# Kernel optimization log

Hardware: AMD Instinct MI355X
Metric: run time of the kernel (lower is better)

## Reference

```python
import jax, jax.numpy as jnp
import numpy as np

INPUT_SIZE = 1024  # enc_dim + dec_dim after concat
ENC_DIM = 512
DEC_DIM = 512
INNER_DIM = 512
VOCAB = 2048


def setup_inputs() -> dict:
    key = jax.random.key(0)
    k1, k2, k3, k4, k5, k6 = jax.random.split(key, 6)
    B, T, U = 4, 256, 128
    enc_state = jax.random.normal(k1, (B, T, ENC_DIM), dtype=jnp.float32)
    dec_state = jax.random.normal(k2, (B, U, DEC_DIM), dtype=jnp.float32)
    # forward_layer: Linear(input_size, inner_dim); stored as [in, out] for jax
    s1 = 1.0 / np.sqrt(INPUT_SIZE)
    W1 = jax.random.uniform(k3, (INPUT_SIZE, INNER_DIM), jnp.float32, -s1, s1)
    b1 = jax.random.uniform(k4, (INNER_DIM,), jnp.float32, -s1, s1)
    s2 = 1.0 / np.sqrt(INNER_DIM)
    W2 = jax.random.uniform(k5, (INNER_DIM, VOCAB), jnp.float32, -s2, s2)
    b2 = jax.random.uniform(k6, (VOCAB,), jnp.float32, -s2, s2)
    return {"enc_state": enc_state, "dec_state": dec_state,
            "W1": W1, "b1": b1, "W2": W2, "b2": b2}


def reference(enc_state, dec_state, W1, b1, W2, b2):
    # JointNet: concat(enc_repeat, dec_repeat) @ W1 + b1 -> tanh -> @ W2 + b2.
    # Since W1 acts on the concat axis, split it: concat @ W1 == enc @ W1_e + dec @ W1_d
    # (mathematically identical, avoids materializing the [B,T,U,2D] concat tensor).
    W1_enc = W1[:ENC_DIM]   # [D_enc, inner]
    W1_dec = W1[ENC_DIM:]   # [D_dec, inner]
    enc_proj = jnp.einsum('btd,dh->bth', enc_state, W1_enc)  # [B,T,H]
    dec_proj = jnp.einsum('bud,dh->buh', dec_state, W1_dec)  # [B,U,H]
    h = jnp.tanh(enc_proj[:, :, None, :] + dec_proj[:, None, :, :] + b1)  # [B,T,U,H]
    logits = jnp.einsum('btuh,hv->btuv', h, W2) + b2  # [B,T,U,V]
    return logits
```

## Files before the change

kernel.cpp:

```cpp
#include <hip/hip_runtime.h>
#include <hip/hip_bf16.h>


typedef __attribute__((ext_vector_type(4))) float f32x4;
typedef __attribute__((ext_vector_type(8))) __bf16 bf16x8;
typedef __attribute__((ext_vector_type(8))) unsigned short u16x8;

__device__ __forceinline__ float bf2f(unsigned short u) {
  unsigned int x = ((unsigned int)u) << 16;
  return __builtin_bit_cast(float, x);
}
__device__ __forceinline__ unsigned short f2bf(float f) {
  unsigned int x = __builtin_bit_cast(unsigned int, f);
  x += 0x7fff + ((x >> 16) & 1);
  return (unsigned short)(x >> 16);
}
__device__ __forceinline__ float tanh_fast(float x) {
  float e = __expf(2.0f * x);
  return 1.0f - 2.0f * __builtin_amdgcn_rcpf(e + 1.0f);
}

typedef __attribute__((address_space(3))) unsigned int lds_u32;
typedef const __attribute__((address_space(1))) unsigned int glb_u32;
__device__ __forceinline__ void gl16(const void* g, void* l) {
  __builtin_amdgcn_global_load_lds((glb_u32*)g, (lds_u32*)l, 16, 0, 0);
}

#define BAR __builtin_amdgcn_s_barrier()
#define LGKM0 asm volatile("s_waitcnt lgkmcnt(0)" ::: "memory")
#define VMCNT(n) asm volatile("s_waitcnt vmcnt(" #n ")" ::: "memory")
#define MEMPIN asm volatile("" ::: "memory")

__global__ __launch_bounds__(512) void proj8_kernel(
    const float* __restrict__ enc, const float* __restrict__ dec,
    const float* __restrict__ W1, const float* __restrict__ b1,
    float* __restrict__ enc_proj, unsigned short* __restrict__ decb) {
  __shared__ float xs[8][512];
  const int bid = blockIdx.x;
  const bool isenc = bid < 128;
  const int rows0 = (isenc ? bid : bid - 128) * 8;
  const float* src = (isenc ? enc : dec) + (size_t)rows0 * 512;
  const int tid = threadIdx.x;
#pragma unroll
  for (int j = 0; j < 2; ++j) {
    int v = j * 512 + tid;
    int row = v >> 7;
    int c4 = (v & 127) << 2;
    *(f32x4*)&xs[row][c4] = *(const f32x4*)&src[(size_t)row * 512 + c4];
  }
  __syncthreads();
  const int h = tid;
  const float* wp = W1 + (isenc ? 0 : (size_t)512 * 512) + h;
  float acc[8];
  float init = isenc ? 0.f : b1[h];
#pragma unroll
  for (int r = 0; r < 8; ++r) acc[r] = init;
#pragma unroll 4
  for (int k = 0; k < 512; ++k) {
    float wv = wp[(size_t)k * 512];
#pragma unroll
    for (int r = 0; r < 8; ++r) acc[r] = fmaf(xs[r][k], wv, acc[r]);
  }
  if (isenc) {
#pragma unroll
    for (int r = 0; r < 8; ++r) enc_proj[(size_t)(rows0 + r) * 512 + h] = acc[r];
  } else {
#pragma unroll
    for (int r = 0; r < 8; ++r) decb[(size_t)(rows0 + r) * 512 + h] = f2bf(acc[r]);
  }
}

__global__ __launch_bounds__(256) void w2t_kernel(const float* __restrict__ W2,
                                                  unsigned short* __restrict__ W2t) {
  __shared__ unsigned short tile[32][33];
  int bn = blockIdx.x;
  int bk = blockIdx.y;
  int tx = threadIdx.x & 31;
  int ty = threadIdx.x >> 5;
#pragma unroll
  for (int i = 0; i < 32; i += 8)
    tile[ty + i][tx] = f2bf(W2[(size_t)(bk * 32 + ty + i) * 2048 + bn * 32 + tx]);
  __syncthreads();
#pragma unroll
  for (int i = 0; i < 32; i += 8)
    W2t[(size_t)(bn * 32 + ty + i) * 512 + bk * 32 + tx] = tile[tx][ty + i];
}

__global__ __launch_bounds__(256) void h_kernel(
    const float* __restrict__ encp, const unsigned short* __restrict__ decb,
    unsigned short* __restrict__ Hout) {
  int gid = blockIdx.x * 256 + threadIdx.x;
  int m = gid >> 6;
  int hc = (gid & 63) << 3;
  int bt = m >> 7;
  int bu = ((m >> 15) << 7) | (m & 127);
  u16x8 dv = *(const u16x8*)(decb + (size_t)bu * 512 + hc);
  f32x4 e0 = *(const f32x4*)(encp + (size_t)bt * 512 + hc);
  f32x4 e1 = *(const f32x4*)(encp + (size_t)bt * 512 + hc + 4);
  u16x8 hv;
#pragma unroll
  for (int j = 0; j < 4; ++j) hv[j] = f2bf(tanh_fast(bf2f(dv[j]) + e0[j]));
#pragma unroll
  for (int j = 0; j < 4; ++j) hv[4 + j] = f2bf(tanh_fast(bf2f(dv[4 + j]) + e1[j]));
  *(u16x8*)(Hout + (size_t)m * 512 + hc) = hv;
}


__global__ __launch_bounds__(512, 4) void gemm32_kernel(
    const unsigned short* __restrict__ H,
    const unsigned short* __restrict__ W2t,
    const float* __restrict__ b2,
    float* __restrict__ out) {
  __shared__ __align__(1024) char smem[73728];

  const int bid = blockIdx.x;
  const int wg = (bid & 7) * 1024 + (bid >> 3);
  const int my = wg >> 3;
  const int ny = wg & 7;

  const int tid = threadIdx.x;
  const int lane = tid & 63;
  const int w = tid >> 6;
  const int wm = w >> 2;
  const int wn = w & 3;
  const int fr = lane & 15;
  const int fq = lane >> 4;

  const char* ha = (const char*)(H + (size_t)my * 128 * 512);
  const char* wb = (const char*)(W2t + (size_t)ny * 256 * 512);

  size_t srcA, srcB[2];
  {
    int d = w * 1024 + lane * 16;
    int r = d >> 6;
    int c = (d >> 4) & 3;
    srcA = (size_t)r * 1024 + (size_t)((c ^ ((r >> 1) & 3)) << 4);
  }
#pragma unroll
  for (int p = 0; p < 2; ++p) {
    int d = p * 8192 + w * 1024 + lane * 16;
    int r = d >> 6;
    int c = (d >> 4) & 3;
    srcB[p] = (size_t)r * 1024 + (size_t)((c ^ ((r >> 1) & 3)) << 4);
  }

  const int swz = (fq ^ ((fr >> 1) & 3)) << 4;
  const int ldsA = (wm * 64 + fr) * 64 + swz;
  const int ldsB = 8192 + (wn * 64 + fr) * 64 + swz;

  f32x4 acc[4][4];
#pragma unroll
  for (int i = 0; i < 4; ++i)
#pragma unroll
    for (int j = 0; j < 4; ++j) acc[i][j] = (f32x4){0.f, 0.f, 0.f, 0.f};

#define STAGE(tt, slot)                                         \
  do {                                                          \
    char* sl = smem + (slot)*24576;                             \
    gl16(ha + srcA + (tt)*64, sl + w * 1024);                   \
    gl16(wb + srcB[0] + (tt)*64, sl + 8192 + w * 1024);         \
    gl16(wb + srcB[1] + (tt)*64, sl + 16384 + w * 1024);        \
  } while (0)

  STAGE(0, 0);
  STAGE(1, 1);

#pragma unroll
  for (int t = 0; t < 16; ++t) {
    if (t < 15) { VMCNT(3); } else { VMCNT(0); }
    BAR; MEMPIN;
    const char* As = smem + (t % 3) * 24576;
    bf16x8 a4[4], b4[4];
#pragma unroll
    for (int mi = 0; mi < 4; ++mi) a4[mi] = *(const bf16x8*)(As + ldsA + mi * 1024);
#pragma unroll
    for (int ni = 0; ni < 4; ++ni) b4[ni] = *(const bf16x8*)(As + ldsB + ni * 1024);
    if (t + 2 < 16) STAGE(t + 2, (t + 2) % 3);
    LGKM0;
    __builtin_amdgcn_s_setprio(1);
#pragma unroll
    for (int mi = 0; mi < 4; ++mi)
#pragma unroll
      for (int ni = 0; ni < 4; ++ni)
        acc[mi][ni] = __builtin_amdgcn_mfma_f32_16x16x32_bf16(
            a4[mi], b4[ni], acc[mi][ni], 0, 0, 0);
    __builtin_amdgcn_s_setprio(0);
  }
  BAR; MEMPIN;

  float* lbuf = (float*)smem;
  const size_t orow0 = (size_t)my * 128;
  const int ncol0 = ny * 256;
  float bvv[4];
#pragma unroll
  for (int ni = 0; ni < 4; ++ni) bvv[ni] = b2[ncol0 + wn * 64 + ni * 16 + fr];

#pragma unroll
  for (int c = 0; c < 8; ++c) {
    if ((c >> 2) == wm) {
      const int mi = c & 3;
#pragma unroll
      for (int ni = 0; ni < 4; ++ni)
#pragma unroll
        for (int r = 0; r < 4; ++r)
          lbuf[(fq * 4 + r) * 260 + wn * 64 + ni * 16 + fr] =
              acc[mi][ni][r] + bvv[ni];
    }
    LGKM0; BAR; MEMPIN;
#pragma unroll
    for (int rr = 0; rr < 2; ++rr) {
      const int row = w * 2 + rr;
      f32x4 v = *(const f32x4*)&lbuf[row * 260 + lane * 4];
      __builtin_nontemporal_store(
          v, (f32x4*)&out[(orow0 + c * 16 + row) * 2048 + ncol0 + lane * 4]);
    }
    LGKM0; BAR; MEMPIN;
  }
#undef STAGE
}

extern "C" void kernel_launch(void* const* d_in, const int* in_sizes, int n_in,
                              void* d_out, int out_size, void* d_ws, size_t ws_size,
                              hipStream_t stream) {
  const float* enc = (const float*)d_in[0];
  const float* dec = (const float*)d_in[1];
  const float* W1  = (const float*)d_in[2];
  const float* b1  = (const float*)d_in[3];
  const float* W2  = (const float*)d_in[4];
  const float* b2  = (const float*)d_in[5];
  float* out = (float*)d_out;

  char* ws = (char*)d_ws;
  float* enc_proj = (float*)ws;
  unsigned short* decb = (unsigned short*)(ws + (2u << 20));
  unsigned short* W2t  = (unsigned short*)(ws + (2u << 20) + (512u << 10));
  unsigned short* Hbuf = (unsigned short*)(ws + (8u << 20));

  proj8_kernel<<<192, 512, 0, stream>>>(enc, dec, W1, b1, enc_proj, decb);
  w2t_kernel<<<dim3(64, 16), 256, 0, stream>>>(W2, W2t);
  h_kernel<<<32768, 256, 0, stream>>>(enc_proj, decb, Hbuf);
  gemm32_kernel<<<8192, 512, 0, stream>>>(Hbuf, W2t, b2, out);
}
```

Before: 398.7 us.

## Fuse tanh activation into GEMM A-tile production, dropping the H intermediate

Removes the separate h_kernel and the 128 MB bf16 H buffer. The GEMM now builds each A tile in LDS itself: it loads decoder-projection rows from global memory, adds the encoder-projection row cached in LDS, applies tanh, and packs the result to bf16. Register prefetch of the decoder rows is pipelined alongside the existing B-tile async loads, which cuts HBM traffic for writing and re-reading H. In exchange the GEMM's inner loop carries extra transcendental ALU work and register pressure, and the output stores change from nontemporal to regular stores.

```diff
diff --git a/kernel.cpp b/kernel.cpp
--- a/kernel.cpp
+++ b/kernel.cpp
@@ -5,6 +5,7 @@
 typedef __attribute__((ext_vector_type(4))) float f32x4;
 typedef __attribute__((ext_vector_type(8))) __bf16 bf16x8;
 typedef __attribute__((ext_vector_type(8))) unsigned short u16x8;
+typedef __attribute__((ext_vector_type(4))) unsigned int u32x4;
 
 __device__ __forceinline__ float bf2f(unsigned short u) {
   unsigned int x = ((unsigned int)u) << 16;
@@ -18,6 +19,9 @@
 __device__ __forceinline__ float tanh_fast(float x) {
   float e = __expf(2.0f * x);
   return 1.0f - 2.0f * __builtin_amdgcn_rcpf(e + 1.0f);
+}
+__device__ __forceinline__ unsigned int pk2bf(float lo, float hi) {
+  return (unsigned int)f2bf(lo) | ((unsigned int)f2bf(hi) << 16);
 }
 
 typedef __attribute__((address_space(3))) unsigned int lds_u32;
@@ -86,32 +90,14 @@
     W2t[(size_t)(bn * 32 + ty + i) * 512 + bk * 32 + tx] = tile[tx][ty + i];
 }
 
-__global__ __launch_bounds__(256) void h_kernel(
-    const float* __restrict__ encp, const unsigned short* __restrict__ decb,
-    unsigned short* __restrict__ Hout) {
-  int gid = blockIdx.x * 256 + threadIdx.x;
-  int m = gid >> 6;
-  int hc = (gid & 63) << 3;
-  int bt = m >> 7;
-  int bu = ((m >> 15) << 7) | (m & 127);
-  u16x8 dv = *(const u16x8*)(decb + (size_t)bu * 512 + hc);
-  f32x4 e0 = *(const f32x4*)(encp + (size_t)bt * 512 + hc);
-  f32x4 e1 = *(const f32x4*)(encp + (size_t)bt * 512 + hc + 4);
-  u16x8 hv;
-#pragma unroll
-  for (int j = 0; j < 4; ++j) hv[j] = f2bf(tanh_fast(bf2f(dv[j]) + e0[j]));
-#pragma unroll
-  for (int j = 0; j < 4; ++j) hv[4 + j] = f2bf(tanh_fast(bf2f(dv[4 + j]) + e1[j]));
-  *(u16x8*)(Hout + (size_t)m * 512 + hc) = hv;
-}
-
-
-__global__ __launch_bounds__(512, 4) void gemm32_kernel(
-    const unsigned short* __restrict__ H,
+
+__global__ __launch_bounds__(512, 4) void gemmft_kernel(
+    const float* __restrict__ encp,
+    const unsigned short* __restrict__ decb,
     const unsigned short* __restrict__ W2t,
     const float* __restrict__ b2,
     float* __restrict__ out) {
-  __shared__ __align__(1024) char smem[73728];
+  __shared__ __align__(1024) char smem[75776];
 
   const int bid = blockIdx.x;
   const int wg = (bid & 7) * 1024 + (bid >> 3);
@@ -126,16 +112,7 @@
   const int fr = lane & 15;
   const int fq = lane >> 4;
 
-  const char* ha = (const char*)(H + (size_t)my * 128 * 512);
-  const char* wb = (const char*)(W2t + (size_t)ny * 256 * 512);
-
-  size_t srcA, srcB[2];
-  {
-    int d = w * 1024 + lane * 16;
-    int r = d >> 6;
-    int c = (d >> 4) & 3;
-    srcA = (size_t)r * 1024 + (size_t)((c ^ ((r >> 1) & 3)) << 4);
-  }
+  size_t srcB[2];
 #pragma unroll
   for (int p = 0; p < 2; ++p) {
     int d = p * 8192 + w * 1024 + lane * 16;
@@ -143,6 +120,17 @@
     int c = (d >> 4) & 3;
     srcB[p] = (size_t)r * 1024 + (size_t)((c ^ ((r >> 1) & 3)) << 4);
   }
+  const char* wb = (const char*)(W2t + (size_t)ny * 256 * 512);
+
+  const int arow = tid >> 2;
+  const int achk = tid & 3;
+  const int aoff = arow * 64 + ((achk ^ ((arow >> 1) & 3)) << 4);
+  const unsigned short* dp =
+      decb + ((size_t)((my >> 8) * 128 + arow)) * 512 + achk * 8;
+
+  float* encl = (float*)(smem + 73728);
+  if (tid < 128)
+    *(f32x4*)&encl[tid * 4] = *(const f32x4*)&encp[(size_t)my * 512 + tid * 4];
 
   const int swz = (fq ^ ((fr >> 1) & 3)) << 4;
   const int ldsA = (wm * 64 + fr) * 64 + swz;
@@ -154,29 +142,64 @@
 #pragma unroll
     for (int j = 0; j < 4; ++j) acc[i][j] = (f32x4){0.f, 0.f, 0.f, 0.f};
 
-#define STAGE(tt, slot)                                         \
+#define STAGEB(tt, slot)                                        \
   do {                                                          \
     char* sl = smem + (slot)*24576;                             \
-    gl16(ha + srcA + (tt)*64, sl + w * 1024);                   \
     gl16(wb + srcB[0] + (tt)*64, sl + 8192 + w * 1024);         \
     gl16(wb + srcB[1] + (tt)*64, sl + 16384 + w * 1024);        \
   } while (0)
 
-  STAGE(0, 0);
-  STAGE(1, 1);
+#define TANHW(s, dv)                                                        \
+  do {                                                                      \
+    f32x4 e0 = *(const f32x4*)&encl[(s)*32 + achk * 8];                     \
+    f32x4 e1 = *(const f32x4*)&encl[(s)*32 + achk * 8 + 4];                 \
+    float f[8];                                                             \
+    _Pragma("unroll") for (int j = 0; j < 4; ++j)                           \
+        f[j] = tanh_fast(bf2f((dv)[j]) + e0[j]);                            \
+    _Pragma("unroll") for (int j = 0; j < 4; ++j)                           \
+        f[4 + j] = tanh_fast(bf2f((dv)[4 + j]) + e1[j]);                    \
+    u32x4 pk;                                                               \
+    _Pragma("unroll") for (int j = 0; j < 4; ++j)                           \
+        pk[j] = pk2bf(f[2 * j], f[2 * j + 1]);                              \
+    *(u32x4*)(smem + ((s) % 3) * 24576 + aoff) = pk;                        \
+  } while (0)
+
+  STAGEB(0, 0);
+  STAGEB(1, 1);
+  LGKM0;
+  BAR; MEMPIN;
+  {
+    u16x8 d0 = *(const u16x8*)(dp);
+    u16x8 d1 = *(const u16x8*)(dp + 32);
+    MEMPIN;
+    TANHW(0, d0);
+    TANHW(1, d1);
+  }
+  u16x8 decreg[2];
+  decreg[0] = *(const u16x8*)(dp + 2 * 32);
+  MEMPIN;
+  VMCNT(0);
+  LGKM0;
+  BAR; MEMPIN;
 
 #pragma unroll
   for (int t = 0; t < 16; ++t) {
-    if (t < 15) { VMCNT(3); } else { VMCNT(0); }
-    BAR; MEMPIN;
+    if (t > 0) {
+      if (t < 15) { VMCNT(2); } else { VMCNT(0); }
+      BAR; MEMPIN;
+    }
     const char* As = smem + (t % 3) * 24576;
     bf16x8 a4[4], b4[4];
 #pragma unroll
     for (int mi = 0; mi < 4; ++mi) a4[mi] = *(const bf16x8*)(As + ldsA + mi * 1024);
 #pragma unroll
     for (int ni = 0; ni < 4; ++ni) b4[ni] = *(const bf16x8*)(As + ldsB + ni * 1024);
-    if (t + 2 < 16) STAGE(t + 2, (t + 2) % 3);
-    LGKM0;
+
+    if (t <= 12) decreg[(t + 1) & 1] = *(const u16x8*)(dp + (t + 3) * 32);
+    MEMPIN;
+    if (t <= 13) STAGEB(t + 2, (t + 2) % 3);
+    MEMPIN;
+
     __builtin_amdgcn_s_setprio(1);
 #pragma unroll
     for (int mi = 0; mi < 4; ++mi)
@@ -185,8 +208,11 @@
         acc[mi][ni] = __builtin_amdgcn_mfma_f32_16x16x32_bf16(
             a4[mi], b4[ni], acc[mi][ni], 0, 0, 0);
     __builtin_amdgcn_s_setprio(0);
-  }
-  BAR; MEMPIN;
+
+    if (t <= 13) TANHW(t + 2, decreg[t & 1]);
+    LGKM0;
+    if (t == 15) { BAR; MEMPIN; }
+  }
 
   float* lbuf = (float*)smem;
   const size_t orow0 = (size_t)my * 128;
@@ -211,12 +237,12 @@
     for (int rr = 0; rr < 2; ++rr) {
       const int row = w * 2 + rr;
       f32x4 v = *(const f32x4*)&lbuf[row * 260 + lane * 4];
-      __builtin_nontemporal_store(
-          v, (f32x4*)&out[(orow0 + c * 16 + row) * 2048 + ncol0 + lane * 4]);
+      *(f32x4*)&out[(orow0 + c * 16 + row) * 2048 + ncol0 + lane * 4] = v;
     }
     LGKM0; BAR; MEMPIN;
   }
-#undef STAGE
+#undef STAGEB
+#undef TANHW
 }
 
 extern "C" void kernel_launch(void* const* d_in, const int* in_sizes, int n_in,
@@ -234,10 +260,8 @@
   float* enc_proj = (float*)ws;
   unsigned short* decb = (unsigned short*)(ws + (2u << 20));
   unsigned short* W2t  = (unsigned short*)(ws + (2u << 20) + (512u << 10));
-  unsigned short* Hbuf = (unsigned short*)(ws + (8u << 20));
 
   proj8_kernel<<<192, 512, 0, stream>>>(enc, dec, W1, b1, enc_proj, decb);
   w2t_kernel<<<dim3(64, 16), 256, 0, stream>>>(W2, W2t);
-  h_kernel<<<32768, 256, 0, stream>>>(enc_proj, decb, Hbuf);
-  gemm32_kernel<<<8192, 512, 0, stream>>>(Hbuf, W2t, b2, out);
-}
+  gemmft_kernel<<<8192, 512, 0, stream>>>(enc_proj, decb, W2t, b2, out);
+}
```

Result: slower. 508.1 us (+27.4%).
